# Kernel tuning notes

Measured on AMD Instinct MI355X. Metric: run time of the kernel, lower is better.

The kernel has to match this reference:

```python
import jax, jax.numpy as jnp
import numpy as np

N_NODES = 100_000
N_EDGES = 1_000_000
D_NODE = 128
D_EDGE = 128
LN_EPS = 1e-5  # torch LayerNorm default
CNT_EPS = 1e-10


def _layernorm(x, gamma, beta):
    m = x.mean(-1, keepdims=True)
    v = ((x - m) ** 2).mean(-1, keepdims=True)
    return (x - m) / jnp.sqrt(v + LN_EPS) * gamma + beta


def setup_inputs() -> dict:
    key = jax.random.key(0)
    ks = jax.random.split(key, 8)
    node_features = jax.random.normal(ks[0], (N_NODES, D_NODE), jnp.float32)
    edge_features = jax.random.normal(ks[1], (N_EDGES, D_EDGE), jnp.float32)
    edge_index = jax.random.randint(ks[2], (2, N_EDGES), 0, N_NODES, jnp.int32)
    d_in_e = D_EDGE + 2 * D_NODE
    d_in_n = D_NODE + D_EDGE
    We = jax.random.normal(ks[3], (d_in_e, D_EDGE), jnp.float32) * (1.0 / np.sqrt(d_in_e))
    be = jnp.zeros((D_EDGE,), jnp.float32)
    gamma_e = jnp.ones((D_EDGE,), jnp.float32)
    beta_e = jnp.zeros((D_EDGE,), jnp.float32)
    Wn = jax.random.normal(ks[4], (d_in_n, D_NODE), jnp.float32) * (1.0 / np.sqrt(d_in_n))
    bn = jnp.zeros((D_NODE,), jnp.float32)
    gamma_n = jnp.ones((D_NODE,), jnp.float32)
    beta_n = jnp.zeros((D_NODE,), jnp.float32)
    return dict(node_features=node_features, edge_features=edge_features,
                edge_index=edge_index, We=We, be=be, gamma_e=gamma_e, beta_e=beta_e,
                Wn=Wn, bn=bn, gamma_n=gamma_n, beta_n=beta_n)


def reference(node_features, edge_features, edge_index, We, be, gamma_e, beta_e,
              Wn, bn, gamma_n, beta_n):
    src, tgt = edge_index[0], edge_index[1]
    # edge update: gather endpoint node feats, linear + residual + LN
    edge_ctx = jnp.concatenate([edge_features, node_features[src], node_features[tgt]], axis=-1)
    new_edges = _layernorm(edge_features + edge_ctx @ We + be, gamma_e, beta_e)
    # aggregate: mean of incident (new) edge features per node (src and tgt both count)
    N = node_features.shape[0]
    all_nodes = jnp.concatenate([src, tgt])
    all_edges = jnp.concatenate([new_edges, new_edges])
    edge_sum = jax.ops.segment_sum(all_edges, all_nodes, num_segments=N)
    edge_count = jax.ops.segment_sum(jnp.ones((all_nodes.shape[0], 1), new_edges.dtype),
                                     all_nodes, num_segments=N)
    edge_mean = edge_sum / (edge_count + CNT_EPS)
    # node update
    node_ctx = jnp.concatenate([node_features, edge_mean], axis=-1)
    new_nodes = _layernorm(node_features + node_ctx @ Wn + bn, gamma_n, beta_n)
    return new_nodes, new_edges
```

## Files before the change

kernel.cpp:

```cpp
#include <hip/hip_runtime.h>

#define N_NODES 100000
#define N_EDGES 1000000
#define D 128
#define NB ((N_NODES + 255) / 256)
#define LN_EPS 1e-5f
#define CNT_EPS 1e-10f

typedef __bf16 bf16x8 __attribute__((ext_vector_type(8)));
typedef __bf16 bf16x4 __attribute__((ext_vector_type(4)));
typedef float  f32x4  __attribute__((ext_vector_type(4)));

#define ROWRED(v) { v += __shfl_xor(v, 1); v += __shfl_xor(v, 2); \
                    v += __shfl_xor(v, 4); v += __shfl_xor(v, 8); }

#define GLOAD16(g, l) \
    __builtin_amdgcn_global_load_lds( \
        (const __attribute__((address_space(1))) void*)(g), \
        (__attribute__((address_space(3))) void*)(l), 16, 0, 0)

__global__ void prep_w(const float* __restrict__ We, const float* __restrict__ Wn,
                       __bf16* __restrict__ Wt, __bf16* __restrict__ Wtn)
{
    const int t = blockIdx.x * 256 + threadIdx.x;
    if (t < 128 * 384) {
        const int j = t / 384, k = t % 384;
        Wt[t] = (__bf16)(We[(size_t)k * 128 + j] + ((k == j) ? 1.0f : 0.0f));
    } else if (t < 128 * 384 + 128 * 256) {
        const int u = t - 128 * 384;
        const int j = u / 256, k = u % 256;
        Wtn[u] = (__bf16)Wn[(size_t)k * 128 + j];
    }
}

#define ESTAGE(b, kt) { \
    _Pragma("unroll") \
    for (int r = 0; r < 4; ++r) { \
        const float* g = ((kt) < 4) ? baseE[r] + (kt) * 32 \
                       : ((kt) < 8) ? baseS[r] + ((kt) - 4) * 32 \
                                    : baseT[r] + ((kt) - 8) * 32; \
        GLOAD16(g, &Asf[b][(wid * 4 + r) * 256]); \
    } \
    _Pragma("unroll") \
    for (int r = 0; r < 2; ++r) \
        GLOAD16(baseW[r] + (kt) * 32, &Btf[b][(wid * 2 + r) * 512]); }

#define EFRAG_MFMA(b) { \
    bf16x8 afm[2]; \
    _Pragma("unroll") \
    for (int mt = 0; mt < 2; ++mt) { \
        const int row = wid * 32 + mt * 16 + li; \
        const int swz = li & 7; \
        const f32x4 va = *(const f32x4*)&Asf[b][row * 32 + (((lg * 2) ^ swz) << 2)]; \
        const f32x4 vb = *(const f32x4*)&Asf[b][row * 32 + (((lg * 2 + 1) ^ swz) << 2)]; \
        bf16x8 af; \
        af[0] = (__bf16)va[0]; af[1] = (__bf16)va[1]; \
        af[2] = (__bf16)va[2]; af[3] = (__bf16)va[3]; \
        af[4] = (__bf16)vb[0]; af[5] = (__bf16)vb[1]; \
        af[6] = (__bf16)vb[2]; af[7] = (__bf16)vb[3]; \
        afm[mt] = af; \
    } \
    _Pragma("unroll") \
    for (int nt = 0; nt < 8; ++nt) { \
        const int col = nt * 16 + li; \
        const bf16x8 bfr = \
            *(const bf16x8*)&Btf[b][col * 32 + ((lg ^ ((li >> 1) & 3)) << 3)]; \
        acc[0][nt] = __builtin_amdgcn_mfma_f32_16x16x32_bf16(afm[0], bfr, acc[0][nt], 0, 0, 0); \
        acc[1][nt] = __builtin_amdgcn_mfma_f32_16x16x32_bf16(afm[1], bfr, acc[1][nt], 0, 0, 0); \
    } }

__launch_bounds__(256)
__global__ void edge_kernel(const float* __restrict__ nodef,
                            const float* __restrict__ edgef,
                            const int*   __restrict__ eidx,
                            const __bf16* __restrict__ Wt,
                            const float* __restrict__ be,
                            const float* __restrict__ gamma_e,
                            const float* __restrict__ beta_e,
                            float* __restrict__ new_edges,
                            __bf16* __restrict__ sh,
                            int* __restrict__ cnt)
{
    __shared__ float  Asf[2][4096];
    __shared__ __bf16 Btf[2][4096];
    __shared__ int s_src[128], s_tgt[128];

    const int tid = threadIdx.x;
    const int e0  = blockIdx.x * 128;

    if (tid < 128) {
        const int v = eidx[min(e0 + tid, N_EDGES - 1)];
        s_src[tid] = v;
        if (e0 + tid < N_EDGES) atomicAdd(&cnt[v], 1);
    } else {
        const int v = eidx[N_EDGES + min(e0 + tid - 128, N_EDGES - 1)];
        s_tgt[tid - 128] = v;
        if (e0 + tid - 128 < N_EDGES) atomicAdd(&cnt[v], 1);
    }
    __syncthreads();

    const int wid  = tid >> 6;
    const int lane = tid & 63;
    const int li   = lane & 15;
    const int lg   = lane >> 4;

    const float* baseE[4];
    const float* baseS[4];
    const float* baseT[4];
    #pragma unroll
    for (int r = 0; r < 4; ++r) {
        const int idx = (wid * 4 + r) * 64 + lane;
        const int row = idx >> 3;
        const int ch  = idx & 7;
        const int cg  = ch ^ (row & 7);
        const int er  = min(e0 + row, N_EDGES - 1);
        baseE[r] = edgef + (size_t)er * D + cg * 4;
        baseS[r] = nodef + (size_t)s_src[row] * D + cg * 4;
        baseT[r] = nodef + (size_t)s_tgt[row] * D + cg * 4;
    }
    const __bf16* baseW[2];
    #pragma unroll
    for (int r = 0; r < 2; ++r) {
        const int idx = (wid * 2 + r) * 64 + lane;
        const int col = idx >> 2;
        const int ch  = idx & 3;
        const int cg  = ch ^ ((col >> 1) & 3);
        baseW[r] = Wt + (size_t)col * 384 + cg * 8;
    }

    f32x4 acc[2][8];
    const f32x4 zero = {0.f, 0.f, 0.f, 0.f};
    #pragma unroll
    for (int m = 0; m < 2; ++m)
        #pragma unroll
        for (int n = 0; n < 8; ++n) acc[m][n] = zero;

    ESTAGE(0, 0);
    __syncthreads();
    #pragma unroll
    for (int kt = 0; kt < 12; ++kt) {
        const int b = kt & 1;
        if (kt < 11) ESTAGE(b ^ 1, kt + 1);
        EFRAG_MFMA(b);
        if (kt < 11) __syncthreads();
    }

    float g[8], bt_[8], bias[8];
    #pragma unroll
    for (int nt = 0; nt < 8; ++nt) {
        const int col = nt * 16 + li;
        g[nt]    = gamma_e[col];
        bt_[nt]  = beta_e[col];
        bias[nt] = be[col];
    }

    #pragma unroll
    for (int mt = 0; mt < 2; ++mt) {
        #pragma unroll
        for (int r = 0; r < 4; ++r) {
            const int rl = wid * 32 + mt * 16 + lg * 4 + r;
            const int e  = e0 + rl;
            float x[8];
            float s = 0.f;
            #pragma unroll
            for (int nt = 0; nt < 8; ++nt) {
                x[nt] = acc[mt][nt][r] + bias[nt];
                s += x[nt];
            }
            ROWRED(s);
            const float mean = s * 0.0078125f;
            float vs = 0.f;
            #pragma unroll
            for (int nt = 0; nt < 8; ++nt) { const float d_ = x[nt] - mean; vs = fmaf(d_, d_, vs); }
            ROWRED(vs);
            const float rstd = rsqrtf(vs * 0.0078125f + LN_EPS);
            if (e < N_EDGES) {
                const size_t ec = (size_t)e;
                float y[8];
                #pragma unroll
                for (int nt = 0; nt < 8; ++nt)
                    y[nt] = fmaf((x[nt] - mean) * rstd, g[nt], bt_[nt]);
                #pragma unroll
                for (int nt = 0; nt < 8; ++nt)
                    new_edges[ec * D + nt * 16 + li] = y[nt];
                if (sh) {
                    #pragma unroll
                    for (int nt = 0; nt < 8; ++nt)
                        sh[ec * D + nt * 16 + li] = (__bf16)y[nt];
                }
            }
        }
    }
}

#define NSTORE() { \
    bf16x8 a0, a1; \
    a0[0] = (__bf16)v0.x; a0[1] = (__bf16)v0.y; a0[2] = (__bf16)v0.z; a0[3] = (__bf16)v0.w; \
    a0[4] = (__bf16)v1.x; a0[5] = (__bf16)v1.y; a0[6] = (__bf16)v1.z; a0[7] = (__bf16)v1.w; \
    a1[0] = (__bf16)v2.x; a1[1] = (__bf16)v2.y; a1[2] = (__bf16)v2.z; a1[3] = (__bf16)v2.w; \
    a1[4] = (__bf16)v3.x; a1[5] = (__bf16)v3.y; a1[6] = (__bf16)v3.z; a1[7] = (__bf16)v3.w; \
    *(bf16x8*)&NAs[lrow][lhalf * 16]     = a0; \
    *(bf16x8*)&NAs[lrow][lhalf * 16 + 8] = a1; \
    *(bf16x8*)&NBt[lrow][lhalf * 16]     = wb0; \
    *(bf16x8*)&NBt[lrow][lhalf * 16 + 8] = wb1; }

#define NLOAD(kt) { \
    const float* ab = ((kt) < 4) ? nodp + (kt) * 32 : aggp + ((kt) - 4) * 32; \
    v0 = ((const float4*)ab)[0]; v1 = ((const float4*)ab)[1]; \
    v2 = ((const float4*)ab)[2]; v3 = ((const float4*)ab)[3]; \
    wb0 = *(const bf16x8*)(wbp + (kt) * 32); \
    wb1 = *(const bf16x8*)(wbp + (kt) * 32 + 8); }

__launch_bounds__(256)
__global__ void node_kernel(const float* __restrict__ nodef,
                            const __bf16* __restrict__ Wtn,
                            const float* __restrict__ bn,
                            const float* __restrict__ gamma_n,
                            const float* __restrict__ beta_n,
                            const float* __restrict__ edge_mean,
                            float* __restrict__ new_nodes)
{
    __shared__ __bf16 NAs[128][40];
    __shared__ __bf16 NBt[128][40];

    const int tid = threadIdx.x;
    const int n0  = blockIdx.x * 128;

    const int lrow  = tid >> 1;
    const int lhalf = tid & 1;
    const size_t nclamp = (size_t)min(n0 + lrow, N_NODES - 1);

    const float* nodp = nodef     + nclamp * D + lhalf * 16;
    const float* aggp = edge_mean + nclamp * D + lhalf * 16;
    const __bf16* wbp = Wtn + (size_t)lrow * 256 + lhalf * 16;

    const int wid  = tid >> 6;
    const int lane = tid & 63;
    const int li   = lane & 15;
    const int lg   = lane >> 4;
    const int k0   = lg * 8;

    f32x4 acc[2][8];
    const f32x4 zero = {0.f, 0.f, 0.f, 0.f};
    #pragma unroll
    for (int m = 0; m < 2; ++m)
        #pragma unroll
        for (int n = 0; n < 8; ++n) acc[m][n] = zero;

    float4 v0, v1, v2, v3;
    bf16x8 wb0, wb1;

    #pragma unroll
    for (int kt = 0; kt < 8; ++kt) {
        NLOAD(kt);
        __syncthreads();
        NSTORE();
        __syncthreads();
        const bf16x8 af0 = *(const bf16x8*)&NAs[wid * 32 + li][k0];
        const bf16x8 af1 = *(const bf16x8*)&NAs[wid * 32 + 16 + li][k0];
        #pragma unroll
        for (int nt = 0; nt < 8; ++nt) {
            const bf16x8 bfr = *(const bf16x8*)&NBt[nt * 16 + li][k0];
            acc[0][nt] = __builtin_amdgcn_mfma_f32_16x16x32_bf16(af0, bfr, acc[0][nt], 0, 0, 0);
            acc[1][nt] = __builtin_amdgcn_mfma_f32_16x16x32_bf16(af1, bfr, acc[1][nt], 0, 0, 0);
        }
    }

    float g[8], bt_[8], bias[8];
    #pragma unroll
    for (int nt = 0; nt < 8; ++nt) {
        const int col = nt * 16 + li;
        g[nt]    = gamma_n[col];
        bt_[nt]  = beta_n[col];
        bias[nt] = bn[col];
    }

    #pragma unroll
    for (int mt = 0; mt < 2; ++mt) {
        #pragma unroll
        for (int r = 0; r < 4; ++r) {
            const int rl = wid * 32 + mt * 16 + lg * 4 + r;
            const int n  = n0 + rl;
            const size_t nc = (size_t)min(n, N_NODES - 1);
            float x[8];
            float s = 0.f;
            #pragma unroll
            for (int nt = 0; nt < 8; ++nt) {
                x[nt] = acc[mt][nt][r] + bias[nt] + nodef[nc * D + nt * 16 + li];
                s += x[nt];
            }
            ROWRED(s);
            const float mean = s * 0.0078125f;
            float vs = 0.f;
            #pragma unroll
            for (int nt = 0; nt < 8; ++nt) { const float d_ = x[nt] - mean; vs = fmaf(d_, d_, vs); }
            ROWRED(vs);
            const float rstd = rsqrtf(vs * 0.0078125f + LN_EPS);
            if (n < N_NODES) {
                #pragma unroll
                for (int nt = 0; nt < 8; ++nt)
                    new_nodes[nc * D + nt * 16 + li] =
                        fmaf((x[nt] - mean) * rstd, g[nt], bt_[nt]);
            }
        }
    }
}

__global__ void scan1(const int* __restrict__ cnt, int* __restrict__ excl,
                      int* __restrict__ bsum)
{
    const int tid = threadIdx.x, lane = tid & 63, wid = tid >> 6;
    const int i = blockIdx.x * 256 + tid;
    const int v = (i < N_NODES) ? cnt[i] : 0;
    int x = v;
    #pragma unroll
    for (int s = 1; s < 64; s <<= 1) { const int t = __shfl_up(x, s); if (lane >= s) x += t; }
    __shared__ int ws[4], wb[4];
    if (lane == 63) ws[wid] = x;
    __syncthreads();
    if (tid == 0) {
        int run = 0;
        #pragma unroll
        for (int w = 0; w < 4; ++w) { wb[w] = run; run += ws[w]; }
        bsum[blockIdx.x] = run;
    }
    __syncthreads();
    if (i < N_NODES) excl[i] = wb[wid] + x - v;
}

__global__ void scan2(int* __restrict__ bsum, int* __restrict__ offs)
{
    __shared__ int ws[4], wb[4];
    __shared__ int sbase;
    const int tid = threadIdx.x, lane = tid & 63, wid = tid >> 6;
    if (tid == 0) sbase = 0;
    __syncthreads();
    for (int chunk = 0; chunk < NB; chunk += 256) {
        const int i = chunk + tid;
        const int v = (i < NB) ? bsum[i] : 0;
        int x = v;
        #pragma unroll
        for (int s = 1; s < 64; s <<= 1) { const int t = __shfl_up(x, s); if (lane >= s) x += t; }
        if (lane == 63) ws[wid] = x;
        __syncthreads();
        if (tid == 0) {
            int run = sbase;
            #pragma unroll
            for (int w = 0; w < 4; ++w) { wb[w] = run; run += ws[w]; }
            sbase = run;
        }
        __syncthreads();
        if (i < NB) bsum[i] = wb[wid] + x - v;
        __syncthreads();
    }
    if (tid == 0) offs[N_NODES] = sbase;
}

__global__ void scan3(const int* __restrict__ excl, const int* __restrict__ bsum,
                      int* __restrict__ offs, int* __restrict__ cursor)
{
    const int i = blockIdx.x * 256 + threadIdx.x;
    if (i < N_NODES) {
        const int o = excl[i] + bsum[i >> 8];
        offs[i] = o;
        cursor[i] = o;
    }
}

__global__ void fill_kernel(const int* __restrict__ eidx,
                            int* __restrict__ cursor,
                            int* __restrict__ list)
{
    const int i = blockIdx.x * blockDim.x + threadIdx.x;
    if (i < 2 * N_EDGES) {
        const int n   = eidx[i];
        const int pos = atomicAdd(&cursor[n], 1);
        list[pos] = (i < N_EDGES) ? i : i - N_EDGES;
    }
}

template<bool SH>
__launch_bounds__(256)
__global__ void aggregate_kernel(const float* __restrict__ nef,
                                 const __bf16* __restrict__ sh,
                                 const int* __restrict__ offs,
                                 const int* __restrict__ list,
                                 float* __restrict__ edge_mean)
{
    const int lane   = threadIdx.x & 63;
    const int gwave  = (blockIdx.x * 256 + threadIdx.x) >> 6;
    const int nwaves = gridDim.x * 4;

    for (int n = gwave; n < N_NODES; n += nwaves) {
        const int beg = offs[n], end = offs[n + 1];
        float ax0 = 0.f, ay0 = 0.f, ax1 = 0.f, ay1 = 0.f;
        float ax2 = 0.f, ay2 = 0.f, ax3 = 0.f, ay3 = 0.f;
        int j = beg;
        if (SH) {
            const unsigned int* base = (const unsigned int*)sh;
            for (; j + 8 <= end; j += 8) {
                unsigned int u[8];
                #pragma unroll
                for (int q = 0; q < 8; ++q)
                    u[q] = base[(size_t)list[j + q] * 64 + lane];
                ax0 += __uint_as_float(u[0] << 16) + __uint_as_float(u[4] << 16);
                ay0 += __uint_as_float(u[0] & 0xffff0000u) + __uint_as_float(u[4] & 0xffff0000u);
                ax1 += __uint_as_float(u[1] << 16) + __uint_as_float(u[5] << 16);
                ay1 += __uint_as_float(u[1] & 0xffff0000u) + __uint_as_float(u[5] & 0xffff0000u);
                ax2 += __uint_as_float(u[2] << 16) + __uint_as_float(u[6] << 16);
                ay2 += __uint_as_float(u[2] & 0xffff0000u) + __uint_as_float(u[6] & 0xffff0000u);
                ax3 += __uint_as_float(u[3] << 16) + __uint_as_float(u[7] << 16);
                ay3 += __uint_as_float(u[3] & 0xffff0000u) + __uint_as_float(u[7] & 0xffff0000u);
            }
            for (; j < end; ++j) {
                const unsigned int u = base[(size_t)list[j] * 64 + lane];
                ax0 += __uint_as_float(u << 16); ay0 += __uint_as_float(u & 0xffff0000u);
            }
        } else {
            for (; j + 4 <= end; j += 4) {
                const int e0 = list[j], e1 = list[j + 1], e2 = list[j + 2], e3 = list[j + 3];
                const float2 w0 = ((const float2*)(nef + (size_t)e0 * D))[lane];
                const float2 w1 = ((const float2*)(nef + (size_t)e1 * D))[lane];
                const float2 w2 = ((const float2*)(nef + (size_t)e2 * D))[lane];
                const float2 w3 = ((const float2*)(nef + (size_t)e3 * D))[lane];
                ax0 += w0.x; ay0 += w0.y; ax1 += w1.x; ay1 += w1.y;
                ax2 += w2.x; ay2 += w2.y; ax3 += w3.x; ay3 += w3.y;
            }
            for (; j < end; ++j) {
                const float2 w = ((const float2*)(nef + (size_t)list[j] * D))[lane];
                ax0 += w.x; ay0 += w.y;
            }
        }
        const float sx = (ax0 + ax1) + (ax2 + ax3);
        const float sy = (ay0 + ay1) + (ay2 + ay3);
        const float inv = 1.0f / ((float)(end - beg) + CNT_EPS);
        ((float2*)(edge_mean + (size_t)n * D))[lane] = make_float2(sx * inv, sy * inv);
    }
}

extern "C" void kernel_launch(void* const* d_in, const int* in_sizes, int n_in,
                              void* d_out, int out_size, void* d_ws, size_t ws_size,
                              hipStream_t stream) {
    const float* nodef   = (const float*)d_in[0];
    const float* edgef   = (const float*)d_in[1];
    const int*   eidx    = (const int*)d_in[2];
    const float* We      = (const float*)d_in[3];
    const float* be      = (const float*)d_in[4];
    const float* gamma_e = (const float*)d_in[5];
    const float* beta_e  = (const float*)d_in[6];
    const float* Wn      = (const float*)d_in[7];
    const float* bn      = (const float*)d_in[8];
    const float* gamma_n = (const float*)d_in[9];
    const float* beta_n  = (const float*)d_in[10];

    float* new_nodes = (float*)d_out;
    float* new_edges = (float*)d_out + (size_t)N_NODES * D;

    char* p = (char*)d_ws;
    __bf16* Wt  = (__bf16*)p;  p += 128 * 384 * 2;
    __bf16* Wtn = (__bf16*)p;  p += 128 * 256 * 2;
    int* cnt    = (int*)p;     p += (size_t)N_NODES * 4;
    int* excl   = (int*)p;     p += (size_t)N_NODES * 4;
    int* offs   = (int*)p;     p += (size_t)(N_NODES + 2) * 4;
    int* cursor = (int*)p;     p += (size_t)N_NODES * 4;
    int* bsum   = (int*)p;     p += 2048;
    int* list   = (int*)p;     p += (size_t)2 * N_EDGES * 4;
    const size_t base_bytes = (size_t)(p - (char*)d_ws);
    const size_t shadow_bytes = (size_t)N_EDGES * D * 2;
    __bf16* shadow = nullptr;
    if (ws_size >= base_bytes + shadow_bytes) shadow = (__bf16*)p;

    hipMemsetAsync(cnt, 0, (size_t)N_NODES * sizeof(int), stream);

    prep_w<<<320, 256, 0, stream>>>(We, Wn, Wt, Wtn);

    edge_kernel<<<(N_EDGES + 127) / 128, 256, 0, stream>>>(
        nodef, edgef, eidx, Wt, be, gamma_e, beta_e, new_edges, shadow, cnt);

    scan1<<<NB, 256, 0, stream>>>(cnt, excl, bsum);
    scan2<<<1, 256, 0, stream>>>(bsum, offs);
    scan3<<<NB, 256, 0, stream>>>(excl, bsum, offs, cursor);
    fill_kernel<<<(2 * N_EDGES + 255) / 256, 256, 0, stream>>>(eidx, cursor, list);

    if (shadow)
        aggregate_kernel<true><<<2048, 256, 0, stream>>>(new_edges, shadow, offs, list, new_nodes);
    else
        aggregate_kernel<false><<<2048, 256, 0, stream>>>(new_edges, nullptr, offs, list, new_nodes);

    node_kernel<<<(N_NODES + 127) / 128, 256, 0, stream>>>(
        nodef, Wtn, bn, gamma_n, beta_n, new_nodes, new_nodes);
}
```

Baseline: 786.5 us.

## Pipeline node GEMM with async LDS loads and drop scan3 pass

The node kernel's register-staged loads are replaced by the same double-buffered global_load_lds pipeline the edge kernel uses. The residual is folded into the bf16 node weight by adding identity, which removes the separate nodef re-read in the epilogue but rounds the residual to bf16. The scan3 kernel is removed: fill and aggregate compute offsets on the fly from excl+bsum and cnt, using a separate zeroed counter. The edge-count atomics are moved to after the first stage's loads are issued so they overlap with them.

After: 670.6 us. 14.7% less time.

```diff
diff --git a/kernel.cpp b/kernel.cpp
--- a/kernel.cpp
+++ b/kernel.cpp
@@ -29,7 +29,7 @@
     } else if (t < 128 * 384 + 128 * 256) {
         const int u = t - 128 * 384;
         const int j = u / 256, k = u % 256;
-        Wtn[u] = (__bf16)Wn[(size_t)k * 128 + j];
+        Wtn[u] = (__bf16)(Wn[(size_t)k * 128 + j] + ((k == j) ? 1.0f : 0.0f));
     }
 }
 
@@ -89,13 +89,9 @@
     const int e0  = blockIdx.x * 128;
 
     if (tid < 128) {
-        const int v = eidx[min(e0 + tid, N_EDGES - 1)];
-        s_src[tid] = v;
-        if (e0 + tid < N_EDGES) atomicAdd(&cnt[v], 1);
+        s_src[tid] = eidx[min(e0 + tid, N_EDGES - 1)];
     } else {
-        const int v = eidx[N_EDGES + min(e0 + tid - 128, N_EDGES - 1)];
-        s_tgt[tid - 128] = v;
-        if (e0 + tid - 128 < N_EDGES) atomicAdd(&cnt[v], 1);
+        s_tgt[tid - 128] = eidx[N_EDGES + min(e0 + tid - 128, N_EDGES - 1)];
     }
     __syncthreads();
 
@@ -136,6 +132,11 @@
         for (int n = 0; n < 8; ++n) acc[m][n] = zero;
 
     ESTAGE(0, 0);
+    if (tid < 128) {
+        if (e0 + tid < N_EDGES) atomicAdd(&cnt[s_src[tid]], 1);
+    } else {
+        if (e0 + tid - 128 < N_EDGES) atomicAdd(&cnt[s_tgt[tid - 128]], 1);
+    }
     __syncthreads();
     #pragma unroll
     for (int kt = 0; kt < 12; ++kt) {
@@ -193,23 +194,16 @@
     }
 }
 
-#define NSTORE() { \
-    bf16x8 a0, a1; \
-    a0[0] = (__bf16)v0.x; a0[1] = (__bf16)v0.y; a0[2] = (__bf16)v0.z; a0[3] = (__bf16)v0.w; \
-    a0[4] = (__bf16)v1.x; a0[5] = (__bf16)v1.y; a0[6] = (__bf16)v1.z; a0[7] = (__bf16)v1.w; \
-    a1[0] = (__bf16)v2.x; a1[1] = (__bf16)v2.y; a1[2] = (__bf16)v2.z; a1[3] = (__bf16)v2.w; \
-    a1[4] = (__bf16)v3.x; a1[5] = (__bf16)v3.y; a1[6] = (__bf16)v3.z; a1[7] = (__bf16)v3.w; \
-    *(bf16x8*)&NAs[lrow][lhalf * 16]     = a0; \
-    *(bf16x8*)&NAs[lrow][lhalf * 16 + 8] = a1; \
-    *(bf16x8*)&NBt[lrow][lhalf * 16]     = wb0; \
-    *(bf16x8*)&NBt[lrow][lhalf * 16 + 8] = wb1; }
-
-#define NLOAD(kt) { \
-    const float* ab = ((kt) < 4) ? nodp + (kt) * 32 : aggp + ((kt) - 4) * 32; \
-    v0 = ((const float4*)ab)[0]; v1 = ((const float4*)ab)[1]; \
-    v2 = ((const float4*)ab)[2]; v3 = ((const float4*)ab)[3]; \
-    wb0 = *(const bf16x8*)(wbp + (kt) * 32); \
-    wb1 = *(const bf16x8*)(wbp + (kt) * 32 + 8); }
+#define NSTAGE(b, kt) { \
+    _Pragma("unroll") \
+    for (int r = 0; r < 4; ++r) { \
+        const float* g = ((kt) < 4) ? baseN[r] + (kt) * 32 \
+                                    : baseM[r] + ((kt) - 4) * 32; \
+        GLOAD16(g, &Asf[b][(wid * 4 + r) * 256]); \
+    } \
+    _Pragma("unroll") \
+    for (int r = 0; r < 2; ++r) \
+        GLOAD16(baseW[r] + (kt) * 32, &Btf[b][(wid * 2 + r) * 512]); }
 
 __launch_bounds__(256)
 __global__ void node_kernel(const float* __restrict__ nodef,
@@ -220,25 +214,38 @@
                             const float* __restrict__ edge_mean,
                             float* __restrict__ new_nodes)
 {
-    __shared__ __bf16 NAs[128][40];
-    __shared__ __bf16 NBt[128][40];
+    __shared__ float  Asf[2][4096];
+    __shared__ __bf16 Btf[2][4096];
 
     const int tid = threadIdx.x;
     const int n0  = blockIdx.x * 128;
-
-    const int lrow  = tid >> 1;
-    const int lhalf = tid & 1;
-    const size_t nclamp = (size_t)min(n0 + lrow, N_NODES - 1);
-
-    const float* nodp = nodef     + nclamp * D + lhalf * 16;
-    const float* aggp = edge_mean + nclamp * D + lhalf * 16;
-    const __bf16* wbp = Wtn + (size_t)lrow * 256 + lhalf * 16;
 
     const int wid  = tid >> 6;
     const int lane = tid & 63;
     const int li   = lane & 15;
     const int lg   = lane >> 4;
-    const int k0   = lg * 8;
+
+    const float* baseN[4];
+    const float* baseM[4];
+    #pragma unroll
+    for (int r = 0; r < 4; ++r) {
+        const int idx = (wid * 4 + r) * 64 + lane;
+        const int row = idx >> 3;
+        const int ch  = idx & 7;
+        const int cg  = ch ^ (row & 7);
+        const size_t nr = (size_t)min(n0 + row, N_NODES - 1);
+        baseN[r] = nodef     + nr * D + cg * 4;
+        baseM[r] = edge_mean + nr * D + cg * 4;
+    }
+    const __bf16* baseW[2];
+    #pragma unroll
+    for (int r = 0; r < 2; ++r) {
+        const int idx = (wid * 2 + r) * 64 + lane;
+        const int col = idx >> 2;
+        const int ch  = idx & 3;
+        const int cg  = ch ^ ((col >> 1) & 3);
+        baseW[r] = Wtn + (size_t)col * 256 + cg * 8;
+    }
 
     f32x4 acc[2][8];
     const f32x4 zero = {0.f, 0.f, 0.f, 0.f};
@@ -247,23 +254,14 @@
         #pragma unroll
         for (int n = 0; n < 8; ++n) acc[m][n] = zero;
 
-    float4 v0, v1, v2, v3;
-    bf16x8 wb0, wb1;
-
+    NSTAGE(0, 0);
+    __syncthreads();
     #pragma unroll
     for (int kt = 0; kt < 8; ++kt) {
-        NLOAD(kt);
-        __syncthreads();
-        NSTORE();
-        __syncthreads();
-        const bf16x8 af0 = *(const bf16x8*)&NAs[wid * 32 + li][k0];
-        const bf16x8 af1 = *(const bf16x8*)&NAs[wid * 32 + 16 + li][k0];
-        #pragma unroll
-        for (int nt = 0; nt < 8; ++nt) {
-            const bf16x8 bfr = *(const bf16x8*)&NBt[nt * 16 + li][k0];
-            acc[0][nt] = __builtin_amdgcn_mfma_f32_16x16x32_bf16(af0, bfr, acc[0][nt], 0, 0, 0);
-            acc[1][nt] = __builtin_amdgcn_mfma_f32_16x16x32_bf16(af1, bfr, acc[1][nt], 0, 0, 0);
-        }
+        const int b = kt & 1;
+        if (kt < 7) NSTAGE(b ^ 1, kt + 1);
+        EFRAG_MFMA(b);
+        if (kt < 7) __syncthreads();
     }
 
     float g[8], bt_[8], bias[8];
@@ -281,12 +279,11 @@
         for (int r = 0; r < 4; ++r) {
             const int rl = wid * 32 + mt * 16 + lg * 4 + r;
             const int n  = n0 + rl;
-            const size_t nc = (size_t)min(n, N_NODES - 1);
             float x[8];
             float s = 0.f;
             #pragma unroll
             for (int nt = 0; nt < 8; ++nt) {
-                x[nt] = acc[mt][nt][r] + bias[nt] + nodef[nc * D + nt * 16 + li];
+                x[nt] = acc[mt][nt][r] + bias[nt];
                 s += x[nt];
             }
             ROWRED(s);
@@ -299,7 +296,7 @@
             if (n < N_NODES) {
                 #pragma unroll
                 for (int nt = 0; nt < 8; ++nt)
-                    new_nodes[nc * D + nt * 16 + li] =
+                    new_nodes[(size_t)n * D + nt * 16 + li] =
                         fmaf((x[nt] - mean) * rstd, g[nt], bt_[nt]);
             }
         }
@@ -328,7 +325,7 @@
     if (i < N_NODES) excl[i] = wb[wid] + x - v;
 }
 
-__global__ void scan2(int* __restrict__ bsum, int* __restrict__ offs)
+__global__ void scan2(int* __restrict__ bsum)
 {
     __shared__ int ws[4], wb[4];
     __shared__ int sbase;
@@ -353,28 +350,18 @@
         if (i < NB) bsum[i] = wb[wid] + x - v;
         __syncthreads();
     }
-    if (tid == 0) offs[N_NODES] = sbase;
-}
-
-__global__ void scan3(const int* __restrict__ excl, const int* __restrict__ bsum,
-                      int* __restrict__ offs, int* __restrict__ cursor)
-{
-    const int i = blockIdx.x * 256 + threadIdx.x;
-    if (i < N_NODES) {
-        const int o = excl[i] + bsum[i >> 8];
-        offs[i] = o;
-        cursor[i] = o;
-    }
 }
 
 __global__ void fill_kernel(const int* __restrict__ eidx,
-                            int* __restrict__ cursor,
+                            const int* __restrict__ excl,
+                            const int* __restrict__ bsum,
+                            int* __restrict__ ctr,
                             int* __restrict__ list)
 {
     const int i = blockIdx.x * blockDim.x + threadIdx.x;
     if (i < 2 * N_EDGES) {
         const int n   = eidx[i];
-        const int pos = atomicAdd(&cursor[n], 1);
+        const int pos = excl[n] + bsum[n >> 8] + atomicAdd(&ctr[n], 1);
         list[pos] = (i < N_EDGES) ? i : i - N_EDGES;
     }
 }
@@ -383,7 +370,9 @@
 __launch_bounds__(256)
 __global__ void aggregate_kernel(const float* __restrict__ nef,
                                  const __bf16* __restrict__ sh,
-                                 const int* __restrict__ offs,
+                                 const int* __restrict__ excl,
+                                 const int* __restrict__ bsum,
+                                 const int* __restrict__ cnt,
                                  const int* __restrict__ list,
                                  float* __restrict__ edge_mean)
 {
@@ -392,7 +381,9 @@
     const int nwaves = gridDim.x * 4;
 
     for (int n = gwave; n < N_NODES; n += nwaves) {
-        const int beg = offs[n], end = offs[n + 1];
+        const int beg = excl[n] + bsum[n >> 8];
+        const int deg = cnt[n];
+        const int end = beg + deg;
         float ax0 = 0.f, ay0 = 0.f, ax1 = 0.f, ay1 = 0.f;
         float ax2 = 0.f, ay2 = 0.f, ax3 = 0.f, ay3 = 0.f;
         int j = beg;
@@ -433,7 +424,7 @@
         }
         const float sx = (ax0 + ax1) + (ax2 + ax3);
         const float sy = (ay0 + ay1) + (ay2 + ay3);
-        const float inv = 1.0f / ((float)(end - beg) + CNT_EPS);
+        const float inv = 1.0f / ((float)deg + CNT_EPS);
         ((float2*)(edge_mean + (size_t)n * D))[lane] = make_float2(sx * inv, sy * inv);
     }
 }
@@ -461,8 +452,7 @@
     __bf16* Wtn = (__bf16*)p;  p += 128 * 256 * 2;
     int* cnt    = (int*)p;     p += (size_t)N_NODES * 4;
     int* excl   = (int*)p;     p += (size_t)N_NODES * 4;
-    int* offs   = (int*)p;     p += (size_t)(N_NODES + 2) * 4;
-    int* cursor = (int*)p;     p += (size_t)N_NODES * 4;
+    int* ctr    = (int*)p;     p += (size_t)N_NODES * 4;
     int* bsum   = (int*)p;     p += 2048;
     int* list   = (int*)p;     p += (size_t)2 * N_EDGES * 4;
     const size_t base_bytes = (size_t)(p - (char*)d_ws);
@@ -471,6 +461,7 @@
     if (ws_size >= base_bytes + shadow_bytes) shadow = (__bf16*)p;
 
     hipMemsetAsync(cnt, 0, (size_t)N_NODES * sizeof(int), stream);
+    hipMemsetAsync(ctr, 0, (size_t)N_NODES * sizeof(int), stream);
 
     prep_w<<<320, 256, 0, stream>>>(We, Wn, Wt, Wtn);
 
@@ -478,14 +469,13 @@
         nodef, edgef, eidx, Wt, be, gamma_e, beta_e, new_edges, shadow, cnt);
 
     scan1<<<NB, 256, 0, stream>>>(cnt, excl, bsum);
-    scan2<<<1, 256, 0, stream>>>(bsum, offs);
-    scan3<<<NB, 256, 0, stream>>>(excl, bsum, offs, cursor);
-    fill_kernel<<<(2 * N_EDGES + 255) / 256, 256, 0, stream>>>(eidx, cursor, list);
+    scan2<<<1, 256, 0, stream>>>(bsum);
+    fill_kernel<<<(2 * N_EDGES + 255) / 256, 256, 0, stream>>>(eidx, excl, bsum, ctr, list);
 
     if (shadow)
-        aggregate_kernel<true><<<2048, 256, 0, stream>>>(new_edges, shadow, offs, list, new_nodes);
+        aggregate_kernel<true><<<2048, 256, 0, stream>>>(new_edges, shadow, excl, bsum, cnt, list, new_nodes);
     else
-        aggregate_kernel<false><<<2048, 256, 0, stream>>>(new_edges, nullptr, offs, list, new_nodes);
+        aggregate_kernel<false><<<2048, 256, 0, stream>>>(new_edges, nullptr, excl, bsum, cnt, list, new_nodes);
 
     node_kernel<<<(N_NODES + 127) / 128, 256, 0, stream>>>(
         nodef, Wtn, bn, gamma_n, beta_n, new_nodes, new_nodes);
```
